# Performance work log

Measured on AMD Instinct MI355X. Metric: run time of the kernel, lower is better.

## Reference

```python
import jax, jax.numpy as jnp
import numpy as np

N_NODES = 50_000
N_EDGES = 1_600_000
N_VMS = 10_000
N_SCORE = 1_000_000
D_IN, D_E, D_OUT = 128, 64, 64
MLP_IN, MLP_H, MLP_OUT = 64, 128, 64
H1, H2 = 50, 25  # GNNTower fixed hidden widths


def setup_inputs() -> dict:
    key = jax.random.key(0)
    ks = jax.random.split(key, 24)
    w = lambda k, s: (jax.random.normal(k, s, jnp.float32) * 0.05)
    return {
        "component_features": jax.random.normal(ks[0], (N_NODES, D_IN), jnp.float32),
        "component_edges_features": jax.random.normal(ks[1], (N_EDGES, D_E), jnp.float32),
        "vm_features": jax.random.normal(ks[2], (N_VMS, MLP_IN), jnp.float32),
        "src": jax.random.randint(ks[3], (N_EDGES,), 0, N_NODES, jnp.int32),
        "dst": jax.random.randint(ks[4], (N_EDGES,), 0, N_NODES, jnp.int32),
        "e_comp": jax.random.randint(ks[5], (N_SCORE,), 0, N_NODES, jnp.int32),
        "e_vm": jax.random.randint(ks[6], (N_SCORE,), 0, N_VMS, jnp.int32),
        # GNN layer 1: W_msg [D_IN+D_E, H1], W_apply [D_IN+H1, H1]
        "Wm1": w(ks[7], (D_IN + D_E, H1)), "bm1": jnp.zeros((H1,), jnp.float32),
        "Wa1": w(ks[8], (D_IN + H1, H1)), "ba1": jnp.zeros((H1,), jnp.float32),
        # GNN layer 2
        "Wm2": w(ks[9], (H1 + D_E, H2)), "bm2": jnp.zeros((H2,), jnp.float32),
        "Wa2": w(ks[10], (H1 + H2, H2)), "ba2": jnp.zeros((H2,), jnp.float32),
        # GNN layer 3
        "Wm3": w(ks[11], (H2 + D_E, D_OUT)), "bm3": jnp.zeros((D_OUT,), jnp.float32),
        "Wa3": w(ks[12], (H2 + D_OUT, D_OUT)), "ba3": jnp.zeros((D_OUT,), jnp.float32),
        # MLP tower
        "Wmlp1": w(ks[13], (MLP_IN, MLP_H)), "bmlp1": jnp.zeros((MLP_H,), jnp.float32),
        "Wmlp2": w(ks[14], (MLP_H, MLP_OUT)), "bmlp2": jnp.zeros((MLP_OUT,), jnp.float32),
    }


def reference(component_features, component_edges_features, vm_features,
              src, dst, e_comp, e_vm,
              Wm1, bm1, Wa1, ba1, Wm2, bm2, Wa2, ba2, Wm3, bm3, Wa3, ba3,
              Wmlp1, bmlp1, Wmlp2, bmlp2):
    ef = component_edges_features

    def gnn_layer(h, Wm, bm, Wa, ba):
        d = h.shape[-1]
        # message: relu(W_msg @ concat(h[src], efeat)) == gather + split matmul (avoids concat copy)
        m = jax.nn.relu(h[src] @ Wm[:d] + ef @ Wm[d:] + bm)  # [E, out]
        # scatter-sum aggregation into destination nodes
        h_neigh = jax.ops.segment_sum(m, dst, num_segments=N_NODES)  # [N, out]
        # apply: relu(W_apply @ concat(h, h_neigh))
        return jax.nn.relu(h @ Wa[:d] + h_neigh @ Wa[d:] + ba)

    h = gnn_layer(component_features, Wm1, bm1, Wa1, ba1)   # [N, 50]
    h = gnn_layer(h, Wm2, bm2, Wa2, ba2)                    # [N, 25]  (dropout = identity in eval)
    h = gnn_layer(h, Wm3, bm3, Wa3, ba3)                    # [N, D_OUT]

    vm = jax.nn.relu(vm_features @ Wmlp1 + bmlp1) @ Wmlp2 + bmlp2  # [V, MLP_OUT]

    # sum over concat(comp_emb[e_comp], vm_emb[e_vm]) == sum of parts
    scores = jnp.sum(h, axis=-1)[e_comp] + jnp.sum(vm, axis=-1)[e_vm]  # [N_SCORE]
    return jax.nn.sigmoid(scores)
```

## Files before the change

kernel.cpp:

```cpp
#include <hip/hip_runtime.h>

typedef unsigned int uint;
typedef unsigned short ushort;
typedef short bf16x8 __attribute__((ext_vector_type(8)));
typedef float f32x4  __attribute__((ext_vector_type(4)));


__device__ __forceinline__ ushort f2bf(float f) {
    uint u = __float_as_uint(f);
    u += 0x7FFFu + ((u >> 16) & 1u);
    return (ushort)(u >> 16);
}
__device__ __forceinline__ uint cvtpk(float lo, float hi) {
    uint r;
    asm("v_cvt_pk_bf16_f32 %0, %1, %2" : "=v"(r) : "v"(lo), "v"(hi));
    return r;
}

template<int K0, int KP0, int K1, int KP1, int KC, int OUT, int WOUT,
         int NTC, int RPT, int MODE>
__global__ __launch_bounds__(256) void tile_gemm(
    const float* __restrict__ X0, int sx0,
    const float* __restrict__ X1, int sx1,
    const float* __restrict__ Wg, const float* __restrict__ Bg,
    float* __restrict__ Y, int sy, int nR)
{
    constexpr int KPT  = KP0 + KP1;
    constexpr int C4   = KC / 4;
    constexpr int OUTP = 4 * NTC;
    constexpr int NTR  = 256 / NTC;
    constexpr int TR   = NTR * RPT;
    static_assert(TR == 128, "tile must be 128 rows");
    static_assert(KPT % KC == 0, "KC must divide KPT");

    __shared__ float4 Xl[TR * C4];
    __shared__ float4 Wl[KC * NTC];
    __shared__ float  __align__(16) bl[OUTP];

    const int tid = threadIdx.x;
    const int r0  = blockIdx.x * TR;

    for (int idx = tid; idx < OUTP; idx += 256)
        bl[idx] = (Bg != nullptr && idx < OUT) ? Bg[idx] : 0.f;

    const int tc  = tid & (NTC - 1);
    const int tr  = tid / NTC;
    const int key = (RPT * tr) >> 3;

    float4 acc[RPT];
    #pragma unroll
    for (int i = 0; i < RPT; i++) acc[i] = make_float4(0.f, 0.f, 0.f, 0.f);

    for (int kc0 = 0; kc0 < KPT; kc0 += KC) {
        if (kc0 != 0) __syncthreads();
        for (int idx = tid; idx < TR * C4; idx += 256) {
            int r = idx / C4, c = idx - r * C4;
            int col = kc0 + 4 * c;
            int gr = r0 + r;
            float4 v = make_float4(0.f, 0.f, 0.f, 0.f);
            if (gr < nR) {
                if (KP1 == 0 || col < KP0)
                    v = *reinterpret_cast<const float4*>(X0 + (long long)gr * sx0 + col);
                else
                    v = *reinterpret_cast<const float4*>(X1 + (long long)gr * sx1 + (col - KP0));
            }
            int cs = c + ((r >> 3) % C4); if (cs >= C4) cs -= C4;
            Xl[r * C4 + cs] = v;
        }
        for (int idx = tid; idx < KC * OUTP; idx += 256) {
            int kl = idx / OUTP, o = idx - kl * OUTP;
            int k = kc0 + kl;
            float v = 0.f;
            if (o < OUT) {
                if (k < KP0) { if (k < K0) v = Wg[k * OUT + o]; }
                else { int kk = k - KP0; if (kk < K1) v = Wg[(K0 + kk) * OUT + o]; }
            }
            ((float*)Wl)[kl * OUTP + o] = v;
        }
        __syncthreads();

        const int km = key % C4;
        #pragma unroll 4
        for (int k4 = 0; k4 < C4; k4++) {
            int cs = k4 + km; if (cs >= C4) cs -= C4;
            float4 x[RPT];
            #pragma unroll
            for (int i = 0; i < RPT; i++)
                x[i] = Xl[(RPT * tr + i) * C4 + cs];
            #pragma unroll
            for (int kk = 0; kk < 4; kk++) {
                float4 w = Wl[(4 * k4 + kk) * NTC + tc];
                #pragma unroll
                for (int i = 0; i < RPT; i++) {
                    float xs = (kk == 0) ? x[i].x : (kk == 1) ? x[i].y
                             : (kk == 2) ? x[i].z : x[i].w;
                    acc[i].x = fmaf(xs, w.x, acc[i].x);
                    acc[i].y = fmaf(xs, w.y, acc[i].y);
                    acc[i].z = fmaf(xs, w.z, acc[i].z);
                    acc[i].w = fmaf(xs, w.w, acc[i].w);
                }
            }
        }
    }

    const float4 b4 = reinterpret_cast<float4*>(bl)[tc];
    const int o = 4 * tc;

    if (MODE == 0 || MODE == 1) {
        if (o < WOUT) {
            #pragma unroll
            for (int i = 0; i < RPT; i++) {
                int gr = r0 + RPT * tr + i;
                if (gr < nR) {
                    float4 v;
                    v.x = acc[i].x + b4.x; v.y = acc[i].y + b4.y;
                    v.z = acc[i].z + b4.z; v.w = acc[i].w + b4.w;
                    if (MODE == 1) {
                        v.x = fmaxf(v.x, 0.f); v.y = fmaxf(v.y, 0.f);
                        v.z = fmaxf(v.z, 0.f); v.w = fmaxf(v.w, 0.f);
                    }
                    *reinterpret_cast<float4*>(Y + (long long)gr * sy + o) = v;
                }
            }
        }
    } else {
        #pragma unroll
        for (int i = 0; i < RPT; i++) {
            int gr = r0 + RPT * tr + i;
            float s = fmaxf(acc[i].x + b4.x, 0.f) + fmaxf(acc[i].y + b4.y, 0.f)
                    + fmaxf(acc[i].z + b4.z, 0.f) + fmaxf(acc[i].w + b4.w, 0.f);
            #pragma unroll
            for (int off = 1; off < NTC; off <<= 1) s += __shfl_xor(s, off);
            if (tc == 0 && gr < nR) Y[gr] = s;
        }
    }
}

template<int K0, int KP0, int K1, int KP1, int KC, int OUT1, int WOUT1,
         int OUT1P, int SY1, int OUT2, int OUT2P, int SY2,
         int NTC, int RPT, int NTC2, int RPT2>
__global__ __launch_bounds__(256) void fused_apply_pre(
    const float* __restrict__ X0, int sx0,
    const float* __restrict__ X1, int sx1,
    const float* __restrict__ Wa, const float* __restrict__ ba,
    const float* __restrict__ Wm, const float* __restrict__ bm,
    float* __restrict__ Y1, float* __restrict__ Y2, int nR)
{
    constexpr int KPT  = KP0 + KP1;
    constexpr int C4   = KC / 4;
    constexpr int OUTP = 4 * NTC;
    constexpr int NTR  = 256 / NTC;
    constexpr int TR   = NTR * RPT;
    constexpr int BLSZ = (OUTP > OUT2P) ? OUTP : OUT2P;
    static_assert(TR == 128, "tile must be 128 rows");
    static_assert(KPT % KC == 0, "KC must divide KPT");
    static_assert((256 / NTC2) * RPT2 == 128, "phase2 covers 128 rows");
    static_assert(OUT2P == 4 * NTC2, "phase2 col tiling");
    static_assert(128 * OUT1P <= TR * C4 * 4, "Hl fits in Xl");
    static_assert(OUT1 * OUT2P <= KC * NTC * 4, "Wm fits in Wl");

    __shared__ float4 Xl[TR * C4];
    __shared__ float4 Wl[KC * NTC];
    __shared__ float  __align__(16) bl[BLSZ];
    float* Hl = (float*)Xl;

    const int tid = threadIdx.x;
    const int r0  = blockIdx.x * TR;

    for (int idx = tid; idx < OUTP; idx += 256)
        bl[idx] = (idx < OUT1) ? ba[idx] : 0.f;

    const int tc  = tid & (NTC - 1);
    const int tr  = tid / NTC;
    const int key = (RPT * tr) >> 3;

    float4 acc[RPT];
    #pragma unroll
    for (int i = 0; i < RPT; i++) acc[i] = make_float4(0.f, 0.f, 0.f, 0.f);

    for (int kc0 = 0; kc0 < KPT; kc0 += KC) {
        if (kc0 != 0) __syncthreads();
        for (int idx = tid; idx < TR * C4; idx += 256) {
            int r = idx / C4, c = idx - r * C4;
            int col = kc0 + 4 * c;
            int gr = r0 + r;
            float4 v = make_float4(0.f, 0.f, 0.f, 0.f);
            if (gr < nR) {
                if (KP1 == 0 || col < KP0)
                    v = *reinterpret_cast<const float4*>(X0 + (long long)gr * sx0 + col);
                else
                    v = *reinterpret_cast<const float4*>(X1 + (long long)gr * sx1 + (col - KP0));
            }
            int cs = c + ((r >> 3) % C4); if (cs >= C4) cs -= C4;
            Xl[r * C4 + cs] = v;
        }
        for (int idx = tid; idx < KC * OUTP; idx += 256) {
            int kl = idx / OUTP, o = idx - kl * OUTP;
            int k = kc0 + kl;
            float v = 0.f;
            if (o < OUT1) {
                if (k < KP0) { if (k < K0) v = Wa[k * OUT1 + o]; }
                else { int kk = k - KP0; if (kk < K1) v = Wa[(K0 + kk) * OUT1 + o]; }
            }
            ((float*)Wl)[kl * OUTP + o] = v;
        }
        __syncthreads();

        const int km = key % C4;
        #pragma unroll 4
        for (int k4 = 0; k4 < C4; k4++) {
            int cs = k4 + km; if (cs >= C4) cs -= C4;
            float4 x[RPT];
            #pragma unroll
            for (int i = 0; i < RPT; i++)
                x[i] = Xl[(RPT * tr + i) * C4 + cs];
            #pragma unroll
            for (int kk = 0; kk < 4; kk++) {
                float4 w = Wl[(4 * k4 + kk) * NTC + tc];
                #pragma unroll
                for (int i = 0; i < RPT; i++) {
                    float xs = (kk == 0) ? x[i].x : (kk == 1) ? x[i].y
                             : (kk == 2) ? x[i].z : x[i].w;
                    acc[i].x = fmaf(xs, w.x, acc[i].x);
                    acc[i].y = fmaf(xs, w.y, acc[i].y);
                    acc[i].z = fmaf(xs, w.z, acc[i].z);
                    acc[i].w = fmaf(xs, w.w, acc[i].w);
                }
            }
        }
    }

    const float4 b4 = reinterpret_cast<float4*>(bl)[tc];
    const int o = 4 * tc;

    __syncthreads();

    if (o < WOUT1) {
        #pragma unroll
        for (int i = 0; i < RPT; i++) {
            int lr = RPT * tr + i;
            int gr = r0 + lr;
            float4 v;
            v.x = fmaxf(acc[i].x + b4.x, 0.f); v.y = fmaxf(acc[i].y + b4.y, 0.f);
            v.z = fmaxf(acc[i].z + b4.z, 0.f); v.w = fmaxf(acc[i].w + b4.w, 0.f);
            if (gr >= nR) v = make_float4(0.f, 0.f, 0.f, 0.f);
            if (o < OUT1P)
                *reinterpret_cast<float4*>(Hl + lr * OUT1P + o) = v;
            if (gr < nR)
                *reinterpret_cast<float4*>(Y1 + (long long)gr * SY1 + o) = v;
        }
    }
    for (int idx = tid; idx < OUT1 * OUT2P; idx += 256) {
        int k = idx / OUT2P, oc = idx - k * OUT2P;
        ((float*)Wl)[idx] = (oc < OUT2) ? Wm[k * OUT2 + oc] : 0.f;
    }
    for (int idx = tid; idx < OUT2P; idx += 256)
        bl[idx] = (idx < OUT2) ? bm[idx] : 0.f;
    __syncthreads();

    const int tc2 = tid & (NTC2 - 1);
    const int tr2 = tid / NTC2;
    float4 acc2[RPT2];
    #pragma unroll
    for (int i = 0; i < RPT2; i++) acc2[i] = make_float4(0.f, 0.f, 0.f, 0.f);

    #pragma unroll 4
    for (int k = 0; k < OUT1; k++) {
        float4 w = reinterpret_cast<float4*>((float*)Wl)[k * NTC2 + tc2];
        #pragma unroll
        for (int i = 0; i < RPT2; i++) {
            float xs = Hl[(RPT2 * tr2 + i) * OUT1P + k];
            acc2[i].x = fmaf(xs, w.x, acc2[i].x);
            acc2[i].y = fmaf(xs, w.y, acc2[i].y);
            acc2[i].z = fmaf(xs, w.z, acc2[i].z);
            acc2[i].w = fmaf(xs, w.w, acc2[i].w);
        }
    }
    const float4 b2 = reinterpret_cast<float4*>(bl)[tc2];
    #pragma unroll
    for (int i = 0; i < RPT2; i++) {
        int gr = r0 + RPT2 * tr2 + i;
        if (gr < nR) {
            float4 v;
            v.x = acc2[i].x + b2.x; v.y = acc2[i].y + b2.y;
            v.z = acc2[i].z + b2.z; v.w = acc2[i].w + b2.w;
            *reinterpret_cast<float4*>(Y2 + (long long)gr * SY2 + 4 * tc2) = v;
        }
    }
}

struct AFrag { float4 f0, f1, f2, f3; };

__device__ __forceinline__ AFrag proj_load_A(
    const float* __restrict__ ef, const int* __restrict__ perm,
    int r0, int nE, int tid)
{
    int row = tid >> 2;
    int kq  = (tid & 3) << 4;
    int gr  = r0 + row;
    long long e = (gr < nE) ? (long long)perm[gr] : 0;
    const float* p = ef + e * 64 + kq;
    AFrag a;
    a.f0 = *reinterpret_cast<const float4*>(p);
    a.f1 = *reinterpret_cast<const float4*>(p + 4);
    a.f2 = *reinterpret_cast<const float4*>(p + 8);
    a.f3 = *reinterpret_cast<const float4*>(p + 12);
    return a;
}

__device__ __forceinline__ void proj_write_A(ushort* Al, const AFrag& a, int tid)
{
    int row = tid >> 2;
    int kq  = (tid & 3) << 4;
    ushort u[16];
    u[0]=f2bf(a.f0.x); u[1]=f2bf(a.f0.y); u[2]=f2bf(a.f0.z); u[3]=f2bf(a.f0.w);
    u[4]=f2bf(a.f1.x); u[5]=f2bf(a.f1.y); u[6]=f2bf(a.f1.z); u[7]=f2bf(a.f1.w);
    u[8]=f2bf(a.f2.x); u[9]=f2bf(a.f2.y); u[10]=f2bf(a.f2.z); u[11]=f2bf(a.f2.w);
    u[12]=f2bf(a.f3.x); u[13]=f2bf(a.f3.y); u[14]=f2bf(a.f3.z); u[15]=f2bf(a.f3.w);
    int kc0 = ((kq >> 3) + 0) ^ (row & 7);
    int kc1 = ((kq >> 3) + 1) ^ (row & 7);
    *reinterpret_cast<bf16x8*>(&Al[(row << 6) + kc0 * 8]) = *reinterpret_cast<bf16x8*>(u);
    *reinterpret_cast<bf16x8*>(&Al[(row << 6) + kc1 * 8]) = *reinterpret_cast<bf16x8*>(u + 8);
}

__global__ __launch_bounds__(256) void proj_fused(
    const float* __restrict__ ef,
    const float* __restrict__ W1e, const float* __restrict__ W2e,
    const float* __restrict__ W3e, const int* __restrict__ perm,
    ushort* __restrict__ G1, ushort* __restrict__ G2, ushort* __restrict__ G3,
    int nE)
{
    constexpr int NT = 10;
    __shared__ ushort Al[64 * 64];
    __shared__ ushort Bl[NT * 128 * 8];

    const int tid = threadIdx.x;

    for (int idx = tid; idx < NT * 128; idx += 256) {
        int t  = idx >> 7;
        int ks = (idx >> 6) & 1;
        int l  = idx & 63;
        int gp  = t * 16 + (l & 15);
        int kb  = ks * 32 + ((l >> 4) << 3);
        ushort u[8];
        #pragma unroll
        for (int j = 0; j < 8; j++) {
            int k = kb + j;
            float w = 0.f;
            if (gp < 64)      { if (gp < 50) w = W1e[k * 50 + gp]; }
            else if (gp < 96) { int c = gp - 64; if (c < 25) w = W2e[k * 25 + c]; }
            else              { int c = gp - 96; w = W3e[k * 64 + c]; }
            u[j] = f2bf(w);
        }
        *reinterpret_cast<bf16x8*>(&Bl[idx * 8]) = *reinterpret_cast<bf16x8*>(u);
    }

    const int wv = tid >> 6;
    const int l  = tid & 63;
    const int ntiles = (nE + 63) >> 6;

    int tile = blockIdx.x;
    AFrag a;
    if (tile < ntiles) a = proj_load_A(ef, perm, tile << 6, nE, tid);

    for (; tile < ntiles; tile += gridDim.x) {
        const int r0 = tile << 6;
        __syncthreads();
        proj_write_A(Al, a, tid);
        __syncthreads();
        int nxt = tile + gridDim.x;
        if (nxt < ntiles) a = proj_load_A(ef, perm, nxt << 6, nE, tid);

        f32x4 acc[NT];
        #pragma unroll
        for (int t = 0; t < NT; t++) acc[t] = (f32x4){0.f, 0.f, 0.f, 0.f};
        const int rl = wv * 16 + (l & 15);
        #pragma unroll
        for (int ks = 0; ks < 2; ks++) {
            int kch = (ks * 4 + (l >> 4)) ^ (rl & 7);
            bf16x8 av = *reinterpret_cast<const bf16x8*>(&Al[(rl << 6) + kch * 8]);
            #pragma unroll
            for (int t = 0; t < NT; t++) {
                bf16x8 b = *reinterpret_cast<const bf16x8*>(&Bl[((t * 2 + ks) * 64 + l) * 8]);
                acc[t] = __builtin_amdgcn_mfma_f32_16x16x32_bf16(av, b, acc[t], 0, 0, 0);
            }
        }

        const int grpS = (r0 >> 2) + (wv << 2) + (l >> 4);
        const int c = l & 15;
        #pragma unroll
        for (int t = 0; t < NT; t++) {
            uint2 pq;
            pq.x = cvtpk(acc[t][0], acc[t][1]);
            pq.y = cvtpk(acc[t][2], acc[t][3]);
            ushort* Gp; size_t idx;
            if (t < 4)      { Gp = G1; idx = (size_t)grpS * 256 + (t * 16 + c) * 4; }
            else if (t < 6) { Gp = G2; idx = (size_t)grpS * 128 + ((t - 4) * 16 + c) * 4; }
            else            { Gp = G3; idx = (size_t)grpS * 256 + ((t - 6) * 16 + c) * 4; }
            *reinterpret_cast<uint2*>(Gp + idx) = pq;
        }
    }
}

template<int NT, int GS>
__global__ __launch_bounds__(256) void proj_single(
    const float* __restrict__ ef,
    const float* __restrict__ W, int wcols,
    const int* __restrict__ perm, ushort* __restrict__ G, int nE)
{
    __shared__ ushort Al[64 * 64];
    __shared__ ushort Bl[NT * 128 * 8];

    const int tid = threadIdx.x;

    for (int idx = tid; idx < NT * 128; idx += 256) {
        int t  = idx >> 7;
        int ks = (idx >> 6) & 1;
        int l  = idx & 63;
        int col = t * 16 + (l & 15);
        int kb  = ks * 32 + ((l >> 4) << 3);
        ushort u[8];
        #pragma unroll
        for (int j = 0; j < 8; j++) {
            int k = kb + j;
            float w = (col < wcols) ? W[k * wcols + col] : 0.f;
            u[j] = f2bf(w);
        }
        *reinterpret_cast<bf16x8*>(&Bl[idx * 8]) = *reinterpret_cast<bf16x8*>(u);
    }

    const int wv = tid >> 6;
    const int l  = tid & 63;
    const int ntiles = (nE + 63) >> 6;

    int tile = blockIdx.x;
    AFrag a;
    if (tile < ntiles) a = proj_load_A(ef, perm, tile << 6, nE, tid);

    for (; tile < ntiles; tile += gridDim.x) {
        const int r0 = tile << 6;
        __syncthreads();
        proj_write_A(Al, a, tid);
        __syncthreads();
        int nxt = tile + gridDim.x;
        if (nxt < ntiles) a = proj_load_A(ef, perm, nxt << 6, nE, tid);

        f32x4 acc[NT];
        #pragma unroll
        for (int t = 0; t < NT; t++) acc[t] = (f32x4){0.f, 0.f, 0.f, 0.f};
        const int rl = wv * 16 + (l & 15);
        #pragma unroll
        for (int ks = 0; ks < 2; ks++) {
            int kch = (ks * 4 + (l >> 4)) ^ (rl & 7);
            bf16x8 av = *reinterpret_cast<const bf16x8*>(&Al[(rl << 6) + kch * 8]);
            #pragma unroll
            for (int t = 0; t < NT; t++) {
                bf16x8 b = *reinterpret_cast<const bf16x8*>(&Bl[((t * 2 + ks) * 64 + l) * 8]);
                acc[t] = __builtin_amdgcn_mfma_f32_16x16x32_bf16(av, b, acc[t], 0, 0, 0);
            }
        }

        const int grpS = (r0 >> 2) + (wv << 2) + (l >> 4);
        const int c = l & 15;
        #pragma unroll
        for (int t = 0; t < NT; t++) {
            uint2 pq;
            pq.x = cvtpk(acc[t][0], acc[t][1]);
            pq.y = cvtpk(acc[t][2], acc[t][3]);
            size_t idx = (size_t)grpS * (GS * 4) + (t * 16 + c) * 4;
            *reinterpret_cast<uint2*>(G + idx) = pq;
        }
    }
}

template<int NCL, int GS, int SP>
__global__ __launch_bounds__(256) void agg_csr(
    const ushort* __restrict__ G, const int* __restrict__ srcp,
    const int* __restrict__ rowp, const float* __restrict__ P,
    float* __restrict__ ng, int nN)
{
    const int o = threadIdx.x & (NCL - 1);
    const int g = threadIdx.x / NCL;
    const int n = blockIdx.x * (256 / NCL) + g;
    if (n >= nN) return;
    const int s0 = rowp[n], s1 = rowp[n + 1];

    float a[8];
    #pragma unroll
    for (int j = 0; j < 8; j++) a[j] = 0.f;

    if (s0 < s1) {
        const int g0 = s0 >> 2, g1 = (s1 - 1) >> 2;
        for (int grp = g0; grp <= g1; grp++) {
            const ushort* gb = G + (size_t)grp * (GS * 4) + o * 32;
            uint4 c0 = *reinterpret_cast<const uint4*>(gb);
            uint4 c1 = *reinterpret_cast<const uint4*>(gb + 8);
            uint4 c2 = *reinterpret_cast<const uint4*>(gb + 16);
            uint4 c3 = *reinterpret_cast<const uint4*>(gb + 24);
            int4 s4 = *reinterpret_cast<const int4*>(srcp + grp * 4);
            const int rlo = s0 - grp * 4;
            const int rhi = s1 - grp * 4;
            #pragma unroll
            for (int r = 0; r < 4; r++) {
                if (r < rlo || r >= rhi) continue;
                const int s = (r == 0) ? s4.x : (r == 1) ? s4.y : (r == 2) ? s4.z : s4.w;
                const float* pp = P + (size_t)s * SP + o * 8;
                float4 pa = *reinterpret_cast<const float4*>(pp);
                float4 pb = *reinterpret_cast<const float4*>(pp + 4);
                #pragma unroll
                for (int k = 0; k < 8; k++) {
                    uint lo, hi;
                    switch (k) {
                        case 0: lo = c0.x; hi = c0.y; break;
                        case 1: lo = c0.z; hi = c0.w; break;
                        case 2: lo = c1.x; hi = c1.y; break;
                        case 3: lo = c1.z; hi = c1.w; break;
                        case 4: lo = c2.x; hi = c2.y; break;
                        case 5: lo = c2.z; hi = c2.w; break;
                        case 6: lo = c3.x; hi = c3.y; break;
                        default: lo = c3.z; hi = c3.w; break;
                    }
                    const uint q = (r & 2) ? hi : lo;
                    const uint v = (r & 1) ? (q & 0xffff0000u) : (q << 16);
                    const float pv = (k == 0) ? pa.x : (k == 1) ? pa.y
                                   : (k == 2) ? pa.z : (k == 3) ? pa.w
                                   : (k == 4) ? pb.x : (k == 5) ? pb.y
                                   : (k == 6) ? pb.z : pb.w;
                    a[k] += fmaxf(pv + __uint_as_float(v), 0.f);
                }
            }
        }
    }
    float4 w0 = {a[0], a[1], a[2], a[3]}, w1 = {a[4], a[5], a[6], a[7]};
    float* yp = ng + (size_t)n * 64 + o * 8;
    *reinterpret_cast<float4*>(yp)     = w0;
    *reinterpret_cast<float4*>(yp + 4) = w1;
}

__global__ __launch_bounds__(256) void hist_kernel(
    const int* __restrict__ dst, int* __restrict__ deg, int nE)
{
    for (int e = blockIdx.x * 256 + threadIdx.x; e < nE; e += gridDim.x * 256)
        atomicAdd(&deg[dst[e]], 1);
}

__global__ __launch_bounds__(256) void scan_blksum(
    const int* __restrict__ deg, int* __restrict__ bsum, int nN)
{
    const int t = threadIdx.x;
    const int base = blockIdx.x * 1024;
    int s = 0;
    for (int i = t; i < 1024; i += 256) {
        int id = base + i;
        s += (id < nN) ? deg[id] : 0;
    }
    #pragma unroll
    for (int off = 32; off > 0; off >>= 1) s += __shfl_down(s, off);
    __shared__ int w[4];
    if ((t & 63) == 0) w[t >> 6] = s;
    __syncthreads();
    if (t == 0) bsum[blockIdx.x] = w[0] + w[1] + w[2] + w[3];
}

__global__ __launch_bounds__(256) void scan_top(
    int* __restrict__ bsum, int nB, int* __restrict__ rowp, int nN)
{
    const int t = threadIdx.x;
    int v = (t < nB) ? bsum[t] : 0;
    int x = v;
    #pragma unroll
    for (int off = 1; off < 64; off <<= 1) {
        int u = __shfl_up(x, off);
        if ((t & 63) >= off) x += u;
    }
    __shared__ int wsum[4];
    if ((t & 63) == 63) wsum[t >> 6] = x;
    __syncthreads();
    int add = 0;
    #pragma unroll
    for (int i = 0; i < 4; i++) if (i < (t >> 6)) add += wsum[i];
    x += add;
    if (t < nB) bsum[t] = x - v;
    if (t == nB - 1) rowp[nN] = x;
}

__global__ __launch_bounds__(256) void scan_final(
    const int* __restrict__ deg, const int* __restrict__ bsum,
    int* __restrict__ rowp, int nN)
{
    const int t = threadIdx.x;
    const int idx0 = blockIdx.x * 1024 + t * 4;
    int e[4];
    #pragma unroll
    for (int i = 0; i < 4; i++) {
        int id = idx0 + i;
        e[i] = (id < nN) ? deg[id] : 0;
    }
    int tl = e[0] + e[1] + e[2] + e[3];
    int x = tl;
    #pragma unroll
    for (int off = 1; off < 64; off <<= 1) {
        int u = __shfl_up(x, off);
        if ((t & 63) >= off) x += u;
    }
    __shared__ int wsum[4];
    if ((t & 63) == 63) wsum[t >> 6] = x;
    __syncthreads();
    int add = 0;
    #pragma unroll
    for (int i = 0; i < 4; i++) if (i < (t >> 6)) add += wsum[i];
    int run = (x - tl) + add + bsum[blockIdx.x];
    #pragma unroll
    for (int i = 0; i < 4; i++) {
        int id = idx0 + i;
        if (id < nN) rowp[id] = run;
        run += e[i];
    }
}

__global__ __launch_bounds__(256) void scatter_kernel(
    const int* __restrict__ src, const int* __restrict__ dst,
    const int* __restrict__ rowp, int* __restrict__ cursor,
    int* __restrict__ srcp, int* __restrict__ perm, int nE)
{
    for (int e = blockIdx.x * 256 + threadIdx.x; e < nE; e += gridDim.x * 256) {
        int d = dst[e];
        int pos = rowp[d] + atomicAdd(&cursor[d], 1);
        srcp[pos] = src[e];
        perm[pos] = e;
    }
}

__global__ __launch_bounds__(256) void vm_kernel(
    const float* __restrict__ vmf, const float* __restrict__ W1,
    const float* __restrict__ b1, const float* __restrict__ W2,
    const float* __restrict__ b2, float* __restrict__ vm_sum, int nV)
{
    __shared__ float w2s[132];
    const int tid = threadIdx.x;
    if (tid < 128) {
        float s = 0.f;
        for (int o = 0; o < 64; o++) s += W2[tid * 64 + o];
        w2s[tid] = s;
    } else if (tid == 128) {
        float bs = 0.f;
        for (int o = 0; o < 64; o++) bs += b2[o];
        w2s[128] = bs;
    }
    __syncthreads();

    const int lane = tid & 63;
    const int grp  = tid >> 6;
    for (int v = blockIdx.x * 4 + grp; v < nV; v += gridDim.x * 4) {
        const float* vr = vmf + (long long)v * 64;
        float a0 = b1[lane], a1 = b1[lane + 64];
        #pragma unroll 4
        for (int k = 0; k < 64; k += 4) {
            float4 x = *reinterpret_cast<const float4*>(vr + k);
            a0 = fmaf(x.x, W1[(k + 0) * 128 + lane], a0);
            a0 = fmaf(x.y, W1[(k + 1) * 128 + lane], a0);
            a0 = fmaf(x.z, W1[(k + 2) * 128 + lane], a0);
            a0 = fmaf(x.w, W1[(k + 3) * 128 + lane], a0);
            a1 = fmaf(x.x, W1[(k + 0) * 128 + lane + 64], a1);
            a1 = fmaf(x.y, W1[(k + 1) * 128 + lane + 64], a1);
            a1 = fmaf(x.z, W1[(k + 2) * 128 + lane + 64], a1);
            a1 = fmaf(x.w, W1[(k + 3) * 128 + lane + 64], a1);
        }
        float part = fmaxf(a0, 0.f) * w2s[lane] + fmaxf(a1, 0.f) * w2s[lane + 64];
        #pragma unroll
        for (int off = 32; off > 0; off >>= 1) part += __shfl_down(part, off);
        if (lane == 0) vm_sum[v] = part + w2s[128];
    }
}

__global__ __launch_bounds__(256) void score_kernel(
    const int* __restrict__ ec, const int* __restrict__ ev,
    const float* __restrict__ ns, const float* __restrict__ vs,
    float* __restrict__ out, int n)
{
    int i = blockIdx.x * blockDim.x + threadIdx.x;
    if (i < n) {
        float x = ns[ec[i]] + vs[ev[i]];
        out[i] = 1.f / (1.f + expf(-x));
    }
}

extern "C" void kernel_launch(void* const* d_in, const int* in_sizes, int n_in,
                              void* d_out, int out_size, void* d_ws, size_t ws_size,
                              hipStream_t stream)
{
    const float* comp = (const float*)d_in[0];
    const float* ef   = (const float*)d_in[1];
    const float* vmf  = (const float*)d_in[2];
    const int*   src  = (const int*)d_in[3];
    const int*   dst  = (const int*)d_in[4];
    const int*   ecmp = (const int*)d_in[5];
    const int*   evm  = (const int*)d_in[6];
    const float* Wm1 = (const float*)d_in[7];  const float* bm1 = (const float*)d_in[8];
    const float* Wa1 = (const float*)d_in[9];  const float* ba1 = (const float*)d_in[10];
    const float* Wm2 = (const float*)d_in[11]; const float* bm2 = (const float*)d_in[12];
    const float* Wa2 = (const float*)d_in[13]; const float* ba2 = (const float*)d_in[14];
    const float* Wm3 = (const float*)d_in[15]; const float* bm3 = (const float*)d_in[16];
    const float* Wa3 = (const float*)d_in[17]; const float* ba3 = (const float*)d_in[18];
    const float* W1  = (const float*)d_in[19]; const float* b1  = (const float*)d_in[20];
    const float* W2  = (const float*)d_in[21]; const float* b2  = (const float*)d_in[22];

    const int nN = in_sizes[0] / 128;
    const int nE = in_sizes[3];
    const int nV = in_sizes[2] / 64;
    const int nS = in_sizes[5];
    const int nE4 = (nE + 63) & ~63;

    float* ws = (float*)d_ws;
    float* bufA     = ws;
    float* bufB     = bufA + (size_t)nN * 64;
    float* ng       = bufB + (size_t)nN * 64;
    float* node_sum = ng + (size_t)nN * 64;
    float* vm_sum   = node_sum + nN;
    int*   iws      = (int*)(((size_t)(vm_sum + nV) + 15) & ~(size_t)15);
    int*   deg      = iws;
    int*   cursor   = deg + nN;
    int*   rowp     = cursor + nN;
    int*   bsum     = rowp + nN + 1;
    int*   srcp     = (int*)(((size_t)(bsum + 256) + 15) & ~(size_t)15);
    int*   perm     = srcp + nE;
    size_t Goff = (((size_t)((char*)(perm + nE) - (char*)d_ws)) + 255) & ~(size_t)255;
    ushort* G1 = (ushort*)((char*)d_ws + Goff);
    const size_t g1u = (size_t)nE4 * 64, g2u = (size_t)nE4 * 32, g3u = (size_t)nE4 * 64;
    const bool single = (Goff + (g1u + g2u + g3u) * 2) <= ws_size;
    ushort* G2 = single ? (G1 + g1u) : G1;
    ushort* G3 = single ? (G2 + g2u) : G1;

    float* h1 = bufA;
    float* h2 = bufB;
    float* P1 = bufB;
    float* P2 = bufB;
    float* P3 = bufA;

    const float* We1 = Wm1 + 128 * 50;
    const float* We2 = Wm2 + 50 * 25;
    const float* We3 = Wm3 + 25 * 64;

    const int ngrid  = (nN + 127) / 128;
    const int ptiles = nE4 / 64;
    const int pgrid  = ptiles < 2048 ? ptiles : 2048;
    const int a8grid = (nN * 8 + 255) / 256;
    const int a4grid = (nN * 4 + 255) / 256;
    const int sgrid  = (nE + 255) / 256 < 4096 ? (nE + 255) / 256 : 4096;
    const int nB     = (nN + 1023) / 1024;
    const int vgrid  = ((nV + 3) / 4) < 640 ? ((nV + 3) / 4) : 640;

    hipMemsetAsync(deg, 0, (size_t)(2 * nN) * sizeof(int), stream);
    hist_kernel<<<sgrid, 256, 0, stream>>>(dst, deg, nE);
    scan_blksum<<<nB, 256, 0, stream>>>(deg, bsum, nN);
    scan_top<<<1, 256, 0, stream>>>(bsum, nB, rowp, nN);
    scan_final<<<nB, 256, 0, stream>>>(deg, bsum, rowp, nN);
    scatter_kernel<<<sgrid, 256, 0, stream>>>(src, dst, rowp, cursor, srcp, perm, nE);

    if (single)
        proj_fused<<<pgrid, 256, 0, stream>>>(ef, We1, We2, We3, perm, G1, G2, G3, nE);
    else
        proj_single<4, 64><<<pgrid, 256, 0, stream>>>(ef, We1, 50, perm, G1, nE);

    tile_gemm<128,128, 0,0, 64, 50, 64, 16, 8, 0><<<ngrid, 256, 0, stream>>>(
        comp, 128, nullptr, 0, Wm1, bm1, P1, 64, nN);
    agg_csr<8, 64, 64><<<a8grid, 256, 0, stream>>>(G1, srcp, rowp, P1, ng, nN);
    if (!single)
        proj_single<2, 32><<<pgrid, 256, 0, stream>>>(ef, We2, 25, perm, G2, nE);
    fused_apply_pre<128,128, 50,52, 60, 50, 52, 52, 52, 25, 32, 32, 16, 8, 8, 4>
        <<<ngrid, 256, 0, stream>>>(comp, 128, ng, 64, Wa1, ba1, Wm2, bm2, h1, P2, nN);

    agg_csr<4, 32, 32><<<a4grid, 256, 0, stream>>>(G2, srcp, rowp, P2, ng, nN);
    if (!single)
        proj_single<4, 64><<<pgrid, 256, 0, stream>>>(ef, We3, 64, perm, G3, nE);
    fused_apply_pre<50,52, 25,28, 80, 25, 28, 28, 28, 64, 64, 64, 8, 4, 16, 8>
        <<<ngrid, 256, 0, stream>>>(h1, 52, ng, 64, Wa2, ba2, Wm3, bm3, h2, P3, nN);

    agg_csr<8, 64, 64><<<a8grid, 256, 0, stream>>>(G3, srcp, rowp, P3, ng, nN);
    tile_gemm<25,28, 64,68, 48, 64, 64, 16, 8, 2><<<ngrid, 256, 0, stream>>>(
        h2, 28, ng, 64, Wa3, ba3, node_sum, 1, nN);

    vm_kernel<<<vgrid, 256, 0, stream>>>(vmf, W1, b1, W2, b2, vm_sum, nV);
    score_kernel<<<(nS + 255) / 256, 256, 0, stream>>>(ecmp, evm, node_sum, vm_sum, (float*)d_out, nS);
}
```

Baseline: 789.7 us.

## Fuse layer-3 CSR aggregation with apply GEMM and row-sum reduction

Replaces the separate layer-3 aggregation kernel and the final tile_gemm (mode 2) with a single kernel, agg_apply3. Each group of 8 threads aggregates one node's neighbour messages, computes the apply GEMM from shared-memory weights using wave shuffles, and writes the relu row sum directly. This drops the write and reread of the 64-wide neighbour buffer and one launch. In exchange, each thread does more scalar FMA work, the block loads an 89x64 weight tile into shared memory, and the unused reduction mode is removed from tile_gemm.

```diff
diff --git a/kernel.cpp b/kernel.cpp
--- a/kernel.cpp
+++ b/kernel.cpp
@@ -106,32 +106,20 @@
     const float4 b4 = reinterpret_cast<float4*>(bl)[tc];
     const int o = 4 * tc;
 
-    if (MODE == 0 || MODE == 1) {
-        if (o < WOUT) {
-            #pragma unroll
-            for (int i = 0; i < RPT; i++) {
-                int gr = r0 + RPT * tr + i;
-                if (gr < nR) {
-                    float4 v;
-                    v.x = acc[i].x + b4.x; v.y = acc[i].y + b4.y;
-                    v.z = acc[i].z + b4.z; v.w = acc[i].w + b4.w;
-                    if (MODE == 1) {
-                        v.x = fmaxf(v.x, 0.f); v.y = fmaxf(v.y, 0.f);
-                        v.z = fmaxf(v.z, 0.f); v.w = fmaxf(v.w, 0.f);
-                    }
-                    *reinterpret_cast<float4*>(Y + (long long)gr * sy + o) = v;
-                }
-            }
-        }
-    } else {
+    if (o < WOUT) {
         #pragma unroll
         for (int i = 0; i < RPT; i++) {
             int gr = r0 + RPT * tr + i;
-            float s = fmaxf(acc[i].x + b4.x, 0.f) + fmaxf(acc[i].y + b4.y, 0.f)
-                    + fmaxf(acc[i].z + b4.z, 0.f) + fmaxf(acc[i].w + b4.w, 0.f);
-            #pragma unroll
-            for (int off = 1; off < NTC; off <<= 1) s += __shfl_xor(s, off);
-            if (tc == 0 && gr < nR) Y[gr] = s;
+            if (gr < nR) {
+                float4 v;
+                v.x = acc[i].x + b4.x; v.y = acc[i].y + b4.y;
+                v.z = acc[i].z + b4.z; v.w = acc[i].w + b4.w;
+                if (MODE == 1) {
+                    v.x = fmaxf(v.x, 0.f); v.y = fmaxf(v.y, 0.f);
+                    v.z = fmaxf(v.z, 0.f); v.w = fmaxf(v.w, 0.f);
+                }
+                *reinterpret_cast<float4*>(Y + (long long)gr * sy + o) = v;
+            }
         }
     }
 }
@@ -537,6 +525,109 @@
     *reinterpret_cast<float4*>(yp + 4) = w1;
 }
 
+__global__ __launch_bounds__(256) void agg_apply3(
+    const ushort* __restrict__ G, const int* __restrict__ srcp,
+    const int* __restrict__ rowp, const float* __restrict__ P,
+    const float* __restrict__ h2,
+    const float* __restrict__ Wa3, const float* __restrict__ ba3,
+    float* __restrict__ node_sum, int nN)
+{
+    __shared__ float Wl[89 * 64];
+    __shared__ float bl[64];
+    const int tid = threadIdx.x;
+    for (int idx = tid; idx < 89 * 64; idx += 256) Wl[idx] = Wa3[idx];
+    if (tid < 64) bl[tid] = ba3[tid];
+    __syncthreads();
+
+    const int o = tid & 7;
+    const int n = blockIdx.x * 32 + (tid >> 3);
+    if (n >= nN) return;
+    const int s0 = rowp[n], s1 = rowp[n + 1];
+
+    float a[8];
+    #pragma unroll
+    for (int j = 0; j < 8; j++) a[j] = 0.f;
+
+    if (s0 < s1) {
+        const int g0 = s0 >> 2, g1 = (s1 - 1) >> 2;
+        for (int grp = g0; grp <= g1; grp++) {
+            const ushort* gb = G + (size_t)grp * 256 + o * 32;
+            uint4 c0 = *reinterpret_cast<const uint4*>(gb);
+            uint4 c1 = *reinterpret_cast<const uint4*>(gb + 8);
+            uint4 c2 = *reinterpret_cast<const uint4*>(gb + 16);
+            uint4 c3 = *reinterpret_cast<const uint4*>(gb + 24);
+            int4 s4 = *reinterpret_cast<const int4*>(srcp + grp * 4);
+            const int rlo = s0 - grp * 4;
+            const int rhi = s1 - grp * 4;
+            #pragma unroll
+            for (int r = 0; r < 4; r++) {
+                if (r < rlo || r >= rhi) continue;
+                const int s = (r == 0) ? s4.x : (r == 1) ? s4.y : (r == 2) ? s4.z : s4.w;
+                const float* pp = P + (size_t)s * 64 + o * 8;
+                float4 pa = *reinterpret_cast<const float4*>(pp);
+                float4 pb = *reinterpret_cast<const float4*>(pp + 4);
+                #pragma unroll
+                for (int k = 0; k < 8; k++) {
+                    uint lo, hi;
+                    switch (k) {
+                        case 0: lo = c0.x; hi = c0.y; break;
+                        case 1: lo = c0.z; hi = c0.w; break;
+                        case 2: lo = c1.x; hi = c1.y; break;
+                        case 3: lo = c1.z; hi = c1.w; break;
+                        case 4: lo = c2.x; hi = c2.y; break;
+                        case 5: lo = c2.z; hi = c2.w; break;
+                        case 6: lo = c3.x; hi = c3.y; break;
+                        default: lo = c3.z; hi = c3.w; break;
+                    }
+                    const uint q = (r & 2) ? hi : lo;
+                    const uint v = (r & 1) ? (q & 0xffff0000u) : (q << 16);
+                    const float pv = (k == 0) ? pa.x : (k == 1) ? pa.y
+                                   : (k == 2) ? pa.z : (k == 3) ? pa.w
+                                   : (k == 4) ? pb.x : (k == 5) ? pb.y
+                                   : (k == 6) ? pb.z : pb.w;
+                    a[k] += fmaxf(pv + __uint_as_float(v), 0.f);
+                }
+            }
+        }
+    }
+
+    const int o8 = o * 8;
+    float outp[8];
+    #pragma unroll
+    for (int c = 0; c < 8; c++) outp[c] = bl[o8 + c];
+
+    const float* hr = h2 + (size_t)n * 28;
+    for (int k = 0; k < 25; k++) {
+        float hv = hr[k];
+        #pragma unroll
+        for (int c = 0; c < 8; c++)
+            outp[c] = fmaf(hv, Wl[k * 64 + o8 + c], outp[c]);
+    }
+
+    const int lbase = (tid & 63) & ~7;
+    #pragma unroll
+    for (int g = 0; g < 8; g++) {
+        float av[8];
+        #pragma unroll
+        for (int j = 0; j < 8; j++) av[j] = __shfl(a[j], lbase + g, 64);
+        #pragma unroll
+        for (int j = 0; j < 8; j++) {
+            const float* wr = &Wl[(25 + g * 8 + j) * 64 + o8];
+            #pragma unroll
+            for (int c = 0; c < 8; c++)
+                outp[c] = fmaf(av[j], wr[c], outp[c]);
+        }
+    }
+
+    float s = 0.f;
+    #pragma unroll
+    for (int c = 0; c < 8; c++) s += fmaxf(outp[c], 0.f);
+    s += __shfl_xor(s, 1);
+    s += __shfl_xor(s, 2);
+    s += __shfl_xor(s, 4);
+    if (o == 0) node_sum[n] = s;
+}
+
 __global__ __launch_bounds__(256) void hist_kernel(
     const int* __restrict__ dst, int* __restrict__ deg, int nE)
 {
@@ -746,6 +837,7 @@
     const int pgrid  = ptiles < 2048 ? ptiles : 2048;
     const int a8grid = (nN * 8 + 255) / 256;
     const int a4grid = (nN * 4 + 255) / 256;
+    const int aagrid = (nN + 31) / 32;
     const int sgrid  = (nE + 255) / 256 < 4096 ? (nE + 255) / 256 : 4096;
     const int nB     = (nN + 1023) / 1024;
     const int vgrid  = ((nV + 3) / 4) < 640 ? ((nV + 3) / 4) : 640;
@@ -776,9 +868,7 @@
     fused_apply_pre<50,52, 25,28, 80, 25, 28, 28, 28, 64, 64, 64, 8, 4, 16, 8>
         <<<ngrid, 256, 0, stream>>>(h1, 52, ng, 64, Wa2, ba2, Wm3, bm3, h2, P3, nN);
 
-    agg_csr<8, 64, 64><<<a8grid, 256, 0, stream>>>(G3, srcp, rowp, P3, ng, nN);
-    tile_gemm<25,28, 64,68, 48, 64, 64, 16, 8, 2><<<ngrid, 256, 0, stream>>>(
-        h2, 28, ng, 64, Wa3, ba3, node_sum, 1, nN);
+    agg_apply3<<<aagrid, 256, 0, stream>>>(G3, srcp, rowp, P3, h2, Wa3, ba3, node_sum, nN);
 
     vm_kernel<<<vgrid, 256, 0, stream>>>(vmf, W1, b1, W2, b2, vm_sum, nV);
     score_kernel<<<(nS + 255) / 256, 256, 0, stream>>>(ecmp, evm, node_sum, vm_sum, (float*)d_out, nS);
```

Result: faster. 764.5 us (-3.2%).
